# Kernel optimization log

Hardware: AMD Instinct MI355X
Metric: run time of the kernel (lower is better)

Reference implementation:

```python
import jax, jax.numpy as jnp
import numpy as np

EMBED_DIM = 1024
NUM_HEADS = 16
HEAD_DIM = EMBED_DIM // NUM_HEADS
SCALING = HEAD_DIM ** -0.5
TGT_LEN, BSZ = 2048, 2


def setup_inputs() -> dict:
    key = jax.random.key(0)
    k1, k2, k3 = jax.random.split(key, 3)
    return {
        "query": jax.random.normal(k1, (TGT_LEN, BSZ, EMBED_DIM), jnp.float32),
        "in_proj_weight": jax.random.normal(k2, (3 * EMBED_DIM, EMBED_DIM), jnp.float32) * (EMBED_DIM ** -0.5),
        "in_proj_bias": jnp.zeros((3 * EMBED_DIM,), jnp.float32),
        "out_w": jax.random.normal(k3, (EMBED_DIM, EMBED_DIM), jnp.float32) * (EMBED_DIM ** -0.5),
        "out_b": jnp.zeros((EMBED_DIM,), jnp.float32),
    }


def reference(query, in_proj_weight, in_proj_bias, out_w, out_b):
    tgt_len, bsz, embed_dim = query.shape
    # fused QKV projection (self-attention path: qkv_same)
    qkv = query @ in_proj_weight.T + in_proj_bias  # [T, B, 3E]
    q, k, v = jnp.split(qkv, 3, axis=-1)
    q = q * SCALING
    # [T, B, E] -> [B*H, T, hd]
    def to_heads(x):
        return x.reshape(tgt_len, bsz * NUM_HEADS, HEAD_DIM).transpose(1, 0, 2)
    q, k, v = to_heads(q), to_heads(k), to_heads(v)
    attn_weights = jnp.einsum('bqd,bkd->bqk', q, k)          # [B*H, T, T]
    attn_weights = jax.nn.softmax(attn_weights, axis=-1)
    attn = jnp.einsum('bqk,bkd->bqd', attn_weights, v)       # [B*H, T, hd]
    attn = attn.transpose(1, 0, 2).reshape(tgt_len, bsz, embed_dim)
    attn = attn @ out_w.T + out_b
    # averaged attention weights over heads (need_weights=True)
    avg_weights = attn_weights.reshape(bsz, NUM_HEADS, tgt_len, tgt_len).mean(axis=1)
    return attn, avg_weights
```

## Files before the change

kernel.cpp:

```cpp
#include <hip/hip_runtime.h>
#include <hip/hip_bf16.h>
#include <math.h>

#define T_LEN 2048
#define BSZ   2
#define EMB   1024
#define NH    16
#define HD    64
#define BHN   (BSZ*NH)
#define M1    (T_LEN*BSZ)
#define SCAL  0.125f
#define QSCALE (0.125f * 1.44269504088896f)

typedef __attribute__((ext_vector_type(8))) short bf16x8;
typedef __attribute__((ext_vector_type(4))) float f32x4;

__device__ inline unsigned short f2bf(float x) {
    union { float f; unsigned u; } v; v.f = x;
    unsigned r = v.u + 0x7FFF + ((v.u >> 16) & 1);
    return (unsigned short)(r >> 16);
}

__device__ inline unsigned pack2bf(float a, float b) {
    union { __hip_bfloat162 h; unsigned u; } v;
    v.h = __float22bfloat162_rn(make_float2(a, b));
    return v.u;
}

__device__ inline float fexp2(float x) {
#if __has_builtin(__builtin_amdgcn_exp2f)
    return __builtin_amdgcn_exp2f(x);
#else
    return exp2f(x);
#endif
}

__device__ inline void async16(const unsigned short* g, unsigned short* l) {
    __builtin_amdgcn_global_load_lds(
        (const __attribute__((address_space(1))) void*)g,
        (__attribute__((address_space(3))) void*)l, 16, 0, 0);
}

__device__ inline unsigned short* swz(unsigned short* base, int r, int c) {
    return base + (((r << 3) + (c ^ (r & 7))) << 3);
}
__device__ inline const unsigned short* swz(const unsigned short* base, int r, int c) {
    return base + (((r << 3) + (c ^ (r & 7))) << 3);
}

__global__ __launch_bounds__(256) void cvt_bf16_kernel(
    const float* __restrict__ src, unsigned short* __restrict__ dst, int n8)
{
    int idx = blockIdx.x * 256 + threadIdx.x;
    if (idx >= n8) return;
    float4 a = reinterpret_cast<const float4*>(src)[idx * 2];
    float4 b = reinterpret_cast<const float4*>(src)[idx * 2 + 1];
    unsigned o[4] = { pack2bf(a.x, a.y), pack2bf(a.z, a.w),
                      pack2bf(b.x, b.y), pack2bf(b.z, b.w) };
    reinterpret_cast<uint4*>(dst)[idx] = *reinterpret_cast<uint4*>(o);
}

__global__ __launch_bounds__(256) void qkv_mfma_kernel(
    const unsigned short* __restrict__ A, const unsigned short* __restrict__ B,
    const float* __restrict__ bias,
    unsigned short* __restrict__ Q16, unsigned short* __restrict__ K16,
    unsigned short* __restrict__ Vt16)
{
    constexpr int BM = 128, BN = 128, BK = 32, K = 1024;
    __shared__ unsigned short As[BM * BK];
    __shared__ unsigned short Bs[BN * BK];
    const int tid = threadIdx.x;
    const int lane = tid & 63, wave = tid >> 6;
    const int quad = lane >> 4, l16 = lane & 15;
    const int wr = wave >> 1, wc = wave & 1;
    const int m0 = blockIdx.x * BM, n0 = blockIdx.y * BN;

    f32x4 zero4 = {0.f, 0.f, 0.f, 0.f};
    f32x4 acc[4][4];
    #pragma unroll
    for (int i = 0; i < 4; ++i)
        #pragma unroll
        for (int j = 0; j < 4; ++j) acc[i][j] = zero4;

    for (int k0 = 0; k0 < K; k0 += BK) {
        __syncthreads();
        #pragma unroll
        for (int t = 0; t < 2; ++t) {
            int c = t * 256 + tid;
            int m = c >> 2, kb = c & 3;
            async16(&A[(size_t)(m0 + m) * K + k0 + kb * 8], &As[c * 8]);
            async16(&B[(size_t)(n0 + m) * K + k0 + kb * 8], &Bs[c * 8]);
        }
        __syncthreads();
        bf16x8 af[4], bfr[4];
        #pragma unroll
        for (int i = 0; i < 4; ++i) {
            af[i]  = *reinterpret_cast<const bf16x8*>(&As[(wr * 64 + i * 16 + l16) * BK + quad * 8]);
            bfr[i] = *reinterpret_cast<const bf16x8*>(&Bs[(wc * 64 + i * 16 + l16) * BK + quad * 8]);
        }
        #pragma unroll
        for (int i = 0; i < 4; ++i)
            #pragma unroll
            for (int j = 0; j < 4; ++j)
                acc[i][j] = __builtin_amdgcn_mfma_f32_16x16x32_bf16(af[i], bfr[j], acc[i][j], 0, 0, 0);
    }

    #pragma unroll
    for (int j = 0; j < 4; ++j) {
        int n = n0 + wc * 64 + j * 16 + l16;
        float bv = bias[n];
        int which = n >> 10;
        int c = n & 1023;
        int h = c >> 6, d = c & 63;
        #pragma unroll
        for (int i = 0; i < 4; ++i) {
            #pragma unroll
            for (int r = 0; r < 4; ++r) {
                int m = m0 + wr * 64 + i * 16 + quad * 4 + r;
                int t = m >> 1, b = m & 1;
                int bh = b * NH + h;
                float v = acc[i][j][r] + bv;
                if (which == 0)      Q16[((size_t)bh * T_LEN + t) * HD + d] = f2bf(v * QSCALE);
                else if (which == 1) K16[((size_t)bh * T_LEN + t) * HD + d] = f2bf(v);
                else                 Vt16[((size_t)bh * HD + d) * T_LEN + t] = f2bf(v);
            }
        }
    }
}

__global__ __launch_bounds__(256) void flash_mfma_kernel(
    const unsigned short* __restrict__ Qb, const unsigned short* __restrict__ Kb,
    const unsigned short* __restrict__ Vt, unsigned short* __restrict__ AO,
    float* __restrict__ Lrow)
{
    __shared__ unsigned short Ks[64 * 64];
    __shared__ unsigned short Vs[64 * 64];
    __shared__ unsigned short Ps[64 * 64];
    const int tid = threadIdx.x;
    const int lane = tid & 63, wave = tid >> 6;
    const int quad = lane >> 4, l16 = lane & 15;
    const int qt = blockIdx.x, bh = blockIdx.y;
    const int q0 = qt * 64;
    const int b = bh >> 4, h = bh & 15;

    const unsigned short* Qp = Qb + ((size_t)bh * T_LEN + q0 + wave * 16 + l16) * HD;
    bf16x8 qf0 = *reinterpret_cast<const bf16x8*>(Qp + quad * 8);
    bf16x8 qf1 = *reinterpret_cast<const bf16x8*>(Qp + 32 + quad * 8);

    f32x4 zero4 = {0.f, 0.f, 0.f, 0.f};
    f32x4 oacc[4] = {zero4, zero4, zero4, zero4};
    float l_i = 0.f;

    const unsigned short* Kbase = Kb + (size_t)bh * T_LEN * HD;
    const unsigned short* Vbase = Vt + (size_t)bh * HD * T_LEN;
    const int Rp = wave * 16 + l16;

    const int cl0 = tid, cl1 = tid + 256;
    const int r0 = cl0 >> 3, c0 = (cl0 & 7) ^ (r0 & 7);
    const int r1 = cl1 >> 3, c1 = (cl1 & 7) ^ (r1 & 7);

    for (int kt = 0; kt < T_LEN; kt += 64) {
        __syncthreads();
        async16(&Kbase[(size_t)(kt + r0) * HD + c0 * 8], &Ks[cl0 * 8]);
        async16(&Kbase[(size_t)(kt + r1) * HD + c1 * 8], &Ks[cl1 * 8]);
        async16(&Vbase[(size_t)r0 * T_LEN + kt + c0 * 8], &Vs[cl0 * 8]);
        async16(&Vbase[(size_t)r1 * T_LEN + kt + c1 * 8], &Vs[cl1 * 8]);
        __syncthreads();

        f32x4 sacc[4] = {zero4, zero4, zero4, zero4};
        #pragma unroll
        for (int kb = 0; kb < 4; ++kb) {
            bf16x8 kf0 = *reinterpret_cast<const bf16x8*>(swz(Ks, kb * 16 + l16, quad));
            sacc[kb] = __builtin_amdgcn_mfma_f32_16x16x32_bf16(kf0, qf0, sacc[kb], 0, 0, 0);
            bf16x8 kf1 = *reinterpret_cast<const bf16x8*>(swz(Ks, kb * 16 + l16, 4 + quad));
            sacc[kb] = __builtin_amdgcn_mfma_f32_16x16x32_bf16(kf1, qf1, sacc[kb], 0, 0, 0);
        }

        float psum = 0.f;
        #pragma unroll
        for (int kb = 0; kb < 4; ++kb) {
            float p0 = fexp2(sacc[kb][0]);
            float p1 = fexp2(sacc[kb][1]);
            float p2 = fexp2(sacc[kb][2]);
            float p3 = fexp2(sacc[kb][3]);
            psum += (p0 + p1) + (p2 + p3);
            unsigned o[2] = { pack2bf(p0, p1), pack2bf(p2, p3) };
            *reinterpret_cast<uint2*>(
                swz(Ps, Rp, 2 * kb + (quad >> 1)) + (quad & 1) * 4) =
                *reinterpret_cast<uint2*>(o);
        }
        psum += __shfl_xor(psum, 16);
        psum += __shfl_xor(psum, 32);
        l_i += psum;

        #pragma unroll
        for (int s = 0; s < 2; ++s) {
            bf16x8 pb = *reinterpret_cast<const bf16x8*>(swz(Ps, Rp, s * 4 + quad));
            #pragma unroll
            for (int dt = 0; dt < 4; ++dt) {
                bf16x8 va = *reinterpret_cast<const bf16x8*>(swz(Vs, dt * 16 + l16, s * 4 + quad));
                oacc[dt] = __builtin_amdgcn_mfma_f32_16x16x32_bf16(va, pb, oacc[dt], 0, 0, 0);
            }
        }
    }

    float rl = 1.0f / l_i;
    int q = q0 + wave * 16 + l16;
    size_t base = ((size_t)q * BSZ + b) * EMB + h * HD;
    #pragma unroll
    for (int dt = 0; dt < 4; ++dt) {
        unsigned o[2] = { pack2bf(oacc[dt][0] * rl, oacc[dt][1] * rl),
                          pack2bf(oacc[dt][2] * rl, oacc[dt][3] * rl) };
        *reinterpret_cast<uint2*>(&AO[base + dt * 16 + quad * 4]) = *reinterpret_cast<uint2*>(o);
    }
    if (quad == 0)
        Lrow[(size_t)bh * T_LEN + q] = l_i;
}

__global__ __launch_bounds__(256) void avg_mfma_kernel(
    const unsigned short* __restrict__ Qb, const unsigned short* __restrict__ Kb,
    const float* __restrict__ Lrow, float* __restrict__ avg_out)
{
    __shared__ unsigned short Ks[64 * 64];
    const int tid = threadIdx.x;
    const int lane = tid & 63, wave = tid >> 6;
    const int quad = lane >> 4, l16 = lane & 15;
    const int kt = blockIdx.x, qt = blockIdx.y, b = blockIdx.z;
    const int q0 = qt * 64, k0 = kt * 64;

    const int cl0 = tid, cl1 = tid + 256;
    const int r0 = cl0 >> 3, c0 = (cl0 & 7) ^ (r0 & 7);
    const int r1 = cl1 >> 3, c1 = (cl1 & 7) ^ (r1 & 7);

    f32x4 zero4 = {0.f, 0.f, 0.f, 0.f};
    f32x4 acc[4] = {zero4, zero4, zero4, zero4};

    for (int h = 0; h < NH; ++h) {
        int bh = b * NH + h;
        __syncthreads();
        const unsigned short* Kg = Kb + ((size_t)bh * T_LEN + k0) * HD;
        async16(&Kg[(size_t)r0 * HD + c0 * 8], &Ks[cl0 * 8]);
        async16(&Kg[(size_t)r1 * HD + c1 * 8], &Ks[cl1 * 8]);
        __syncthreads();

        const unsigned short* Qp = Qb + ((size_t)bh * T_LEN + q0 + wave * 16 + l16) * HD;
        bf16x8 qf0 = *reinterpret_cast<const bf16x8*>(Qp + quad * 8);
        bf16x8 qf1 = *reinterpret_cast<const bf16x8*>(Qp + 32 + quad * 8);

        f32x4 sacc[4] = {zero4, zero4, zero4, zero4};
        #pragma unroll
        for (int c = 0; c < 4; ++c) {
            bf16x8 kb0 = *reinterpret_cast<const bf16x8*>(swz(Ks, c * 16 + l16, quad));
            sacc[c] = __builtin_amdgcn_mfma_f32_16x16x32_bf16(qf0, kb0, sacc[c], 0, 0, 0);
            bf16x8 kb1 = *reinterpret_cast<const bf16x8*>(swz(Ks, c * 16 + l16, 4 + quad));
            sacc[c] = __builtin_amdgcn_mfma_f32_16x16x32_bf16(qf1, kb1, sacc[c], 0, 0, 0);
        }
        #pragma unroll
        for (int r = 0; r < 4; ++r) {
            int q = q0 + wave * 16 + quad * 4 + r;
            float rl = 1.0f / Lrow[(size_t)bh * T_LEN + q];
            #pragma unroll
            for (int c = 0; c < 4; ++c)
                acc[c][r] += fexp2(sacc[c][r]) * rl;
        }
    }
    #pragma unroll
    for (int r = 0; r < 4; ++r) {
        int q = q0 + wave * 16 + quad * 4 + r;
        size_t base = ((size_t)b * T_LEN + q) * T_LEN + k0;
        #pragma unroll
        for (int c = 0; c < 4; ++c)
            avg_out[base + c * 16 + l16] = acc[c][r] * (1.0f / 16.0f);
    }
}

__global__ __launch_bounds__(256) void out_mfma_kernel(
    const unsigned short* __restrict__ A, const unsigned short* __restrict__ B,
    const float* __restrict__ bias, float* __restrict__ out)
{
    constexpr int BM = 128, BN = 128, BK = 32, K = 1024;
    __shared__ unsigned short As[BM * BK];
    __shared__ unsigned short Bs[BN * BK];
    const int tid = threadIdx.x;
    const int lane = tid & 63, wave = tid >> 6;
    const int quad = lane >> 4, l16 = lane & 15;
    const int wr = wave >> 1, wc = wave & 1;
    const int m0 = blockIdx.x * BM, n0 = blockIdx.y * BN;

    f32x4 zero4 = {0.f, 0.f, 0.f, 0.f};
    f32x4 acc[4][4];
    #pragma unroll
    for (int i = 0; i < 4; ++i)
        #pragma unroll
        for (int j = 0; j < 4; ++j) acc[i][j] = zero4;

    for (int k0 = 0; k0 < K; k0 += BK) {
        __syncthreads();
        #pragma unroll
        for (int t = 0; t < 2; ++t) {
            int c = t * 256 + tid;
            int m = c >> 2, kb = c & 3;
            async16(&A[(size_t)(m0 + m) * K + k0 + kb * 8], &As[c * 8]);
            async16(&B[(size_t)(n0 + m) * K + k0 + kb * 8], &Bs[c * 8]);
        }
        __syncthreads();
        bf16x8 af[4], bfr[4];
        #pragma unroll
        for (int i = 0; i < 4; ++i) {
            af[i]  = *reinterpret_cast<const bf16x8*>(&As[(wr * 64 + i * 16 + l16) * BK + quad * 8]);
            bfr[i] = *reinterpret_cast<const bf16x8*>(&Bs[(wc * 64 + i * 16 + l16) * BK + quad * 8]);
        }
        #pragma unroll
        for (int i = 0; i < 4; ++i)
            #pragma unroll
            for (int j = 0; j < 4; ++j)
                acc[i][j] = __builtin_amdgcn_mfma_f32_16x16x32_bf16(af[i], bfr[j], acc[i][j], 0, 0, 0);
    }

    #pragma unroll
    for (int j = 0; j < 4; ++j) {
        int n = n0 + wc * 64 + j * 16 + l16;
        float bv = bias[n];
        #pragma unroll
        for (int i = 0; i < 4; ++i) {
            #pragma unroll
            for (int r = 0; r < 4; ++r) {
                int m = m0 + wr * 64 + i * 16 + quad * 4 + r;
                out[(size_t)m * 1024 + n] = acc[i][j][r] + bv;
            }
        }
    }
}

extern "C" void kernel_launch(void* const* d_in, const int* in_sizes, int n_in,
                              void* d_out, int out_size, void* d_ws, size_t ws_size,
                              hipStream_t stream)
{
    const float* query = (const float*)d_in[0];
    const float* wqkv  = (const float*)d_in[1];
    const float* bqkv  = (const float*)d_in[2];
    const float* wout  = (const float*)d_in[3];
    const float* bout  = (const float*)d_in[4];
    float* out = (float*)d_out;

    char* ws = (char*)d_ws;
    const size_t E_Q   = (size_t)M1 * EMB;
    const size_t E_W   = (size_t)3 * EMB * EMB;
    const size_t E_WO  = (size_t)EMB * EMB;
    const size_t E_QKV = (size_t)BHN * T_LEN * HD;

    unsigned short* queryb = (unsigned short*)ws;
    unsigned short* wqkvb  = queryb + E_Q;
    unsigned short* woutb  = wqkvb + E_W;
    unsigned short* Q16    = woutb + E_WO;
    unsigned short* K16    = Q16 + E_QKV;
    unsigned short* Vt16   = K16 + E_QKV;
    unsigned short* AO16   = Vt16 + E_QKV;
    float* Lr = (float*)(AO16 + E_Q);
    const size_t need = (E_Q + E_W + E_WO + 4 * E_QKV) * 2 + (size_t)BHN * T_LEN * 4;
    if (ws_size < need) return;

    cvt_bf16_kernel<<<(int)(E_Q / 8 / 256), 256, 0, stream>>>(query, queryb, (int)(E_Q / 8));
    cvt_bf16_kernel<<<(int)(E_W / 8 / 256), 256, 0, stream>>>(wqkv, wqkvb, (int)(E_W / 8));
    cvt_bf16_kernel<<<(int)(E_WO / 8 / 256), 256, 0, stream>>>(wout, woutb, (int)(E_WO / 8));

    qkv_mfma_kernel<<<dim3(M1 / 128, 3072 / 128), 256, 0, stream>>>(queryb, wqkvb, bqkv, Q16, K16, Vt16);
    flash_mfma_kernel<<<dim3(T_LEN / 64, BHN), 256, 0, stream>>>(Q16, K16, Vt16, AO16, Lr);
    avg_mfma_kernel<<<dim3(T_LEN / 64, T_LEN / 64, BSZ), 256, 0, stream>>>(Q16, K16, Lr, out + (size_t)M1 * EMB);
    out_mfma_kernel<<<dim3(M1 / 128, 1024 / 128), 256, 0, stream>>>(AO16, woutb, bout, out);
}
```

Before: 256.4 us.

## Double-buffer K/V in attention kernels, keep P in registers, fuse conversions

```diff
diff --git a/kernel.cpp b/kernel.cpp
--- a/kernel.cpp
+++ b/kernel.cpp
@@ -14,6 +14,7 @@
 
 typedef __attribute__((ext_vector_type(8))) short bf16x8;
 typedef __attribute__((ext_vector_type(4))) float f32x4;
+typedef __attribute__((ext_vector_type(2))) unsigned int u32x2;
 
 __device__ inline unsigned short f2bf(float x) {
     union { float f; unsigned u; } v; v.f = x;
@@ -41,6 +42,14 @@
         (__attribute__((address_space(3))) void*)l, 16, 0, 0);
 }
 
+__device__ inline void hard_barrier() {
+    __builtin_amdgcn_sched_barrier(0);
+    asm volatile("" ::: "memory");
+    __builtin_amdgcn_s_barrier();
+    asm volatile("" ::: "memory");
+    __builtin_amdgcn_sched_barrier(0);
+}
+
 __device__ inline unsigned short* swz(unsigned short* base, int r, int c) {
     return base + (((r << 3) + (c ^ (r & 7))) << 3);
 }
@@ -48,16 +57,40 @@
     return base + (((r << 3) + (c ^ (r & 7))) << 3);
 }
 
-__global__ __launch_bounds__(256) void cvt_bf16_kernel(
-    const float* __restrict__ src, unsigned short* __restrict__ dst, int n8)
+__device__ inline void xchg(unsigned e, unsigned o, unsigned& w_lo, unsigned& w_hi) {
+#if __has_builtin(__builtin_amdgcn_permlane32_swap) && __has_builtin(__builtin_amdgcn_permlane16_swap)
+    u32x2 x = __builtin_amdgcn_permlane32_swap(e, o, false, false);
+    u32x2 y = __builtin_amdgcn_permlane16_swap(x[0], x[1], false, false);
+    w_lo = y[0]; w_hi = y[1];
+#else
+    int lane = (int)(threadIdx.x & 63);
+    int quad = lane >> 4, l16 = lane & 15;
+    int srcA = ((quad & 1) * 2) * 16 + l16;
+    int srcB = ((quad & 1) * 2 + 1) * 16 + l16;
+    unsigned ea = (unsigned)__shfl((int)e, srcA, 64);
+    unsigned oa = (unsigned)__shfl((int)o, srcA, 64);
+    unsigned eb = (unsigned)__shfl((int)e, srcB, 64);
+    unsigned ob = (unsigned)__shfl((int)o, srcB, 64);
+    w_lo = (quad >> 1) ? oa : ea;
+    w_hi = (quad >> 1) ? ob : eb;
+#endif
+}
+
+__global__ __launch_bounds__(256) void cvt3_kernel(
+    const float* __restrict__ s0, const float* __restrict__ s1,
+    const float* __restrict__ s2, unsigned short* __restrict__ dst,
+    int n0, int n1)
 {
     int idx = blockIdx.x * 256 + threadIdx.x;
-    if (idx >= n8) return;
-    float4 a = reinterpret_cast<const float4*>(src)[idx * 2];
-    float4 b = reinterpret_cast<const float4*>(src)[idx * 2 + 1];
-    unsigned o[4] = { pack2bf(a.x, a.y), pack2bf(a.z, a.w),
-                      pack2bf(b.x, b.y), pack2bf(b.z, b.w) };
-    reinterpret_cast<uint4*>(dst)[idx] = *reinterpret_cast<uint4*>(o);
+    const float* src; int o;
+    if (idx < n0)           { src = s0; o = idx; }
+    else if (idx < n0 + n1) { src = s1; o = idx - n0; }
+    else                    { src = s2; o = idx - n0 - n1; }
+    float4 a = reinterpret_cast<const float4*>(src)[(size_t)o * 2];
+    float4 c = reinterpret_cast<const float4*>(src)[(size_t)o * 2 + 1];
+    unsigned w[4] = { pack2bf(a.x, a.y), pack2bf(a.z, a.w),
+                      pack2bf(c.x, c.y), pack2bf(c.z, c.w) };
+    reinterpret_cast<uint4*>(dst)[idx] = *reinterpret_cast<uint4*>(w);
 }
 
 __global__ __launch_bounds__(256) void qkv_mfma_kernel(
@@ -133,13 +166,16 @@
     const unsigned short* __restrict__ Vt, unsigned short* __restrict__ AO,
     float* __restrict__ Lrow)
 {
-    __shared__ unsigned short Ks[64 * 64];
-    __shared__ unsigned short Vs[64 * 64];
-    __shared__ unsigned short Ps[64 * 64];
+    __shared__ unsigned short Ks[2][64 * 64];
+    __shared__ unsigned short Vs[2][64 * 64];
     const int tid = threadIdx.x;
     const int lane = tid & 63, wave = tid >> 6;
     const int quad = lane >> 4, l16 = lane & 15;
-    const int qt = blockIdx.x, bh = blockIdx.y;
+
+    const int lin = blockIdx.y * gridDim.x + blockIdx.x;
+    const int xcd = lin & 7, slot = lin >> 3;
+    const int bh = xcd * 4 + (slot >> 5);
+    const int qt = slot & 31;
     const int q0 = qt * 64;
     const int b = bh >> 4, h = bh & 15;
 
@@ -153,30 +189,46 @@
 
     const unsigned short* Kbase = Kb + (size_t)bh * T_LEN * HD;
     const unsigned short* Vbase = Vt + (size_t)bh * HD * T_LEN;
-    const int Rp = wave * 16 + l16;
 
     const int cl0 = tid, cl1 = tid + 256;
     const int r0 = cl0 >> 3, c0 = (cl0 & 7) ^ (r0 & 7);
     const int r1 = cl1 >> 3, c1 = (cl1 & 7) ^ (r1 & 7);
 
+    async16(&Kbase[(size_t)r0 * HD + c0 * 8], &Ks[0][cl0 * 8]);
+    async16(&Kbase[(size_t)r1 * HD + c1 * 8], &Ks[0][cl1 * 8]);
+    async16(&Vbase[(size_t)r0 * T_LEN + c0 * 8], &Vs[0][cl0 * 8]);
+    async16(&Vbase[(size_t)r1 * T_LEN + c1 * 8], &Vs[0][cl1 * 8]);
+
+    int cur = 0;
     for (int kt = 0; kt < T_LEN; kt += 64) {
-        __syncthreads();
-        async16(&Kbase[(size_t)(kt + r0) * HD + c0 * 8], &Ks[cl0 * 8]);
-        async16(&Kbase[(size_t)(kt + r1) * HD + c1 * 8], &Ks[cl1 * 8]);
-        async16(&Vbase[(size_t)r0 * T_LEN + kt + c0 * 8], &Vs[cl0 * 8]);
-        async16(&Vbase[(size_t)r1 * T_LEN + kt + c1 * 8], &Vs[cl1 * 8]);
-        __syncthreads();
+        if (kt + 64 < T_LEN) {
+            const int nb = cur ^ 1, nkt = kt + 64;
+            async16(&Kbase[(size_t)(nkt + r0) * HD + c0 * 8], &Ks[nb][cl0 * 8]);
+            async16(&Kbase[(size_t)(nkt + r1) * HD + c1 * 8], &Ks[nb][cl1 * 8]);
+            async16(&Vbase[(size_t)r0 * T_LEN + nkt + c0 * 8], &Vs[nb][cl0 * 8]);
+            async16(&Vbase[(size_t)r1 * T_LEN + nkt + c1 * 8], &Vs[nb][cl1 * 8]);
+            asm volatile("s_waitcnt vmcnt(4)" ::: "memory");
+        } else {
+            asm volatile("s_waitcnt vmcnt(0)" ::: "memory");
+        }
+        hard_barrier();
+
+        const unsigned short* Kt = Ks[cur];
+        const unsigned short* Vv = Vs[cur];
 
         f32x4 sacc[4] = {zero4, zero4, zero4, zero4};
+        __builtin_amdgcn_s_setprio(1);
         #pragma unroll
         for (int kb = 0; kb < 4; ++kb) {
-            bf16x8 kf0 = *reinterpret_cast<const bf16x8*>(swz(Ks, kb * 16 + l16, quad));
+            bf16x8 kf0 = *reinterpret_cast<const bf16x8*>(swz(Kt, kb * 16 + l16, quad));
             sacc[kb] = __builtin_amdgcn_mfma_f32_16x16x32_bf16(kf0, qf0, sacc[kb], 0, 0, 0);
-            bf16x8 kf1 = *reinterpret_cast<const bf16x8*>(swz(Ks, kb * 16 + l16, 4 + quad));
+            bf16x8 kf1 = *reinterpret_cast<const bf16x8*>(swz(Kt, kb * 16 + l16, 4 + quad));
             sacc[kb] = __builtin_amdgcn_mfma_f32_16x16x32_bf16(kf1, qf1, sacc[kb], 0, 0, 0);
         }
+        __builtin_amdgcn_s_setprio(0);
 
         float psum = 0.f;
+        unsigned dlo[4], dhi[4];
         #pragma unroll
         for (int kb = 0; kb < 4; ++kb) {
             float p0 = fexp2(sacc[kb][0]);
@@ -184,24 +236,37 @@
             float p2 = fexp2(sacc[kb][2]);
             float p3 = fexp2(sacc[kb][3]);
             psum += (p0 + p1) + (p2 + p3);
-            unsigned o[2] = { pack2bf(p0, p1), pack2bf(p2, p3) };
-            *reinterpret_cast<uint2*>(
-                swz(Ps, Rp, 2 * kb + (quad >> 1)) + (quad & 1) * 4) =
-                *reinterpret_cast<uint2*>(o);
+            dlo[kb] = pack2bf(p0, p1);
+            dhi[kb] = pack2bf(p2, p3);
         }
         psum += __shfl_xor(psum, 16);
         psum += __shfl_xor(psum, 32);
         l_i += psum;
 
+        bf16x8 pfrag[2];
         #pragma unroll
         for (int s = 0; s < 2; ++s) {
-            bf16x8 pb = *reinterpret_cast<const bf16x8*>(swz(Ps, Rp, s * 4 + quad));
+            unsigned w0, w1, w2, w3;
+            xchg(dlo[2 * s], dlo[2 * s + 1], w0, w2);
+            xchg(dhi[2 * s], dhi[2 * s + 1], w1, w3);
+            union { bf16x8 v; unsigned u[4]; } P;
+            P.u[0] = w0; P.u[1] = w1; P.u[2] = w2; P.u[3] = w3;
+            pfrag[s] = P.v;
+        }
+
+        __builtin_amdgcn_s_setprio(1);
+        #pragma unroll
+        for (int s = 0; s < 2; ++s) {
             #pragma unroll
             for (int dt = 0; dt < 4; ++dt) {
-                bf16x8 va = *reinterpret_cast<const bf16x8*>(swz(Vs, dt * 16 + l16, s * 4 + quad));
-                oacc[dt] = __builtin_amdgcn_mfma_f32_16x16x32_bf16(va, pb, oacc[dt], 0, 0, 0);
+                bf16x8 va = *reinterpret_cast<const bf16x8*>(swz(Vv, dt * 16 + l16, s * 4 + quad));
+                oacc[dt] = __builtin_amdgcn_mfma_f32_16x16x32_bf16(va, pfrag[s], oacc[dt], 0, 0, 0);
             }
         }
+        __builtin_amdgcn_s_setprio(0);
+
+        hard_barrier();
+        cur ^= 1;
     }
 
     float rl = 1.0f / l_i;
@@ -221,7 +286,7 @@
     const unsigned short* __restrict__ Qb, const unsigned short* __restrict__ Kb,
     const float* __restrict__ Lrow, float* __restrict__ avg_out)
 {
-    __shared__ unsigned short Ks[64 * 64];
+    __shared__ unsigned short Ks[2][64 * 64];
     const int tid = threadIdx.x;
     const int lane = tid & 63, wave = tid >> 6;
     const int quad = lane >> 4, l16 = lane & 15;
@@ -235,26 +300,40 @@
     f32x4 zero4 = {0.f, 0.f, 0.f, 0.f};
     f32x4 acc[4] = {zero4, zero4, zero4, zero4};
 
+    {
+        const unsigned short* Kg = Kb + ((size_t)(b * NH) * T_LEN + k0) * HD;
+        async16(&Kg[(size_t)r0 * HD + c0 * 8], &Ks[0][cl0 * 8]);
+        async16(&Kg[(size_t)r1 * HD + c1 * 8], &Ks[0][cl1 * 8]);
+    }
+
+    int cur = 0;
     for (int h = 0; h < NH; ++h) {
         int bh = b * NH + h;
-        __syncthreads();
-        const unsigned short* Kg = Kb + ((size_t)bh * T_LEN + k0) * HD;
-        async16(&Kg[(size_t)r0 * HD + c0 * 8], &Ks[cl0 * 8]);
-        async16(&Kg[(size_t)r1 * HD + c1 * 8], &Ks[cl1 * 8]);
-        __syncthreads();
-
         const unsigned short* Qp = Qb + ((size_t)bh * T_LEN + q0 + wave * 16 + l16) * HD;
         bf16x8 qf0 = *reinterpret_cast<const bf16x8*>(Qp + quad * 8);
         bf16x8 qf1 = *reinterpret_cast<const bf16x8*>(Qp + 32 + quad * 8);
 
+        if (h + 1 < NH) {
+            const unsigned short* Kg = Kb + ((size_t)(bh + 1) * T_LEN + k0) * HD;
+            int nb = cur ^ 1;
+            async16(&Kg[(size_t)r0 * HD + c0 * 8], &Ks[nb][cl0 * 8]);
+            async16(&Kg[(size_t)r1 * HD + c1 * 8], &Ks[nb][cl1 * 8]);
+            asm volatile("s_waitcnt vmcnt(4)" ::: "memory");
+        } else {
+            asm volatile("s_waitcnt vmcnt(2)" ::: "memory");
+        }
+        hard_barrier();
+
         f32x4 sacc[4] = {zero4, zero4, zero4, zero4};
+        __builtin_amdgcn_s_setprio(1);
         #pragma unroll
         for (int c = 0; c < 4; ++c) {
-            bf16x8 kb0 = *reinterpret_cast<const bf16x8*>(swz(Ks, c * 16 + l16, quad));
+            bf16x8 kb0 = *reinterpret_cast<const bf16x8*>(swz(Ks[cur], c * 16 + l16, quad));
             sacc[c] = __builtin_amdgcn_mfma_f32_16x16x32_bf16(qf0, kb0, sacc[c], 0, 0, 0);
-            bf16x8 kb1 = *reinterpret_cast<const bf16x8*>(swz(Ks, c * 16 + l16, 4 + quad));
+            bf16x8 kb1 = *reinterpret_cast<const bf16x8*>(swz(Ks[cur], c * 16 + l16, 4 + quad));
             sacc[c] = __builtin_amdgcn_mfma_f32_16x16x32_bf16(qf1, kb1, sacc[c], 0, 0, 0);
         }
+        __builtin_amdgcn_s_setprio(0);
         #pragma unroll
         for (int r = 0; r < 4; ++r) {
             int q = q0 + wave * 16 + quad * 4 + r;
@@ -263,6 +342,8 @@
             for (int c = 0; c < 4; ++c)
                 acc[c][r] += fexp2(sacc[c][r]) * rl;
         }
+        hard_barrier();
+        cur ^= 1;
     }
     #pragma unroll
     for (int r = 0; r < 4; ++r) {
@@ -360,9 +441,8 @@
     const size_t need = (E_Q + E_W + E_WO + 4 * E_QKV) * 2 + (size_t)BHN * T_LEN * 4;
     if (ws_size < need) return;
 
-    cvt_bf16_kernel<<<(int)(E_Q / 8 / 256), 256, 0, stream>>>(query, queryb, (int)(E_Q / 8));
-    cvt_bf16_kernel<<<(int)(E_W / 8 / 256), 256, 0, stream>>>(wqkv, wqkvb, (int)(E_W / 8));
-    cvt_bf16_kernel<<<(int)(E_WO / 8 / 256), 256, 0, stream>>>(wout, woutb, (int)(E_WO / 8));
+    cvt3_kernel<<<(int)((E_Q + E_W + E_WO) / 8 / 256), 256, 0, stream>>>(
+        query, wqkv, wout, queryb, (int)(E_Q / 8), (int)(E_W / 8));
 
     qkv_mfma_kernel<<<dim3(M1 / 128, 3072 / 128), 256, 0, stream>>>(queryb, wqkvb, bqkv, Q16, K16, Vt16);
     flash_mfma_kernel<<<dim3(T_LEN / 64, BHN), 256, 0, stream>>>(Q16, K16, Vt16, AO16, Lr);
```

After: 259.9 us. Within noise of the previous version (+1.4%).
